# Optimization experiments

Hardware: AMD Instinct MI355X
Metric: run time of the kernel (lower is better)

The kernel has to match this reference:

```python
import jax, jax.numpy as jnp
import numpy as np

B, S, D, H = 2, 4096, 512, 8
HD = D // H
SCALE = HD ** -0.5


def setup_inputs() -> dict:
    key = jax.random.key(0)
    ks = jax.random.split(key, 11)
    std = D ** -0.5
    return {
        "query": jax.random.normal(ks[0], (B, S, D), jnp.float32),
        "key":   jax.random.normal(ks[1], (B, S, D), jnp.float32),
        "value": jax.random.normal(ks[2], (B, S, D), jnp.float32),
        "wq": jax.random.normal(ks[3], (D, D), jnp.float32) * std,
        "bq": jnp.zeros((D,), jnp.float32),
        "wk": jax.random.normal(ks[4], (D, D), jnp.float32) * std,
        "bk": jnp.zeros((D,), jnp.float32),
        "wv": jax.random.normal(ks[5], (D, D), jnp.float32) * std,
        "bv": jnp.zeros((D,), jnp.float32),
        "wo": jax.random.normal(ks[6], (D, D), jnp.float32) * std,
        "bo": jnp.zeros((D,), jnp.float32),
    }


def reference(query, key, value, wq, bq, wk, bk, wv, bv, wo, bo):
    # projections: [B,S,D] -> [B,H,S,HD]
    def split_heads(x):
        return x.reshape(B, S, H, HD).transpose(0, 2, 1, 3)

    q = split_heads(query @ wq + bq)
    k = split_heads(key @ wk + bk)
    v = split_heads(value @ wv + bv)

    # full O(S^2) score matrix, as in the original naive MHA
    scores = jnp.einsum("bhqd,bhkd->bhqk", q, k) * SCALE  # [B,H,S,S]
    attn_weights = jax.nn.softmax(scores, axis=-1)
    attn_output = jnp.einsum("bhqk,bhkd->bhqd", attn_weights, v)
    attn_output = attn_output.transpose(0, 2, 1, 3).reshape(B, S, D)
    attn_output = attn_output @ wo + bo
    return attn_output, attn_weights
```

## Files before the change

### kernel.cpp

```cpp
#include <hip/hip_runtime.h>
#include <hip/hip_bf16.h>
#include <cstdint>
#include <cstddef>

#define B_  2
#define S_  4096
#define D_  512
#define H_  8
#define HD_ 64
#define QSCALE_ 0.18033688f

typedef short s16x8 __attribute__((ext_vector_type(8)));
typedef float f32x4 __attribute__((ext_vector_type(4)));

__device__ __forceinline__ unsigned short f2bf(float f) {
    unsigned u = __builtin_bit_cast(unsigned, f);
    u += 0x7fffu + ((u >> 16) & 1u);
    return (unsigned short)(u >> 16);
}

__device__ __forceinline__ unsigned packbf2(float a, float b) {
    unsigned r;
    asm("v_cvt_pk_bf16_f32 %0, %1, %2" : "=v"(r) : "v"(a), "v"(b));
    return r;
}

__device__ __forceinline__ void gload16(const unsigned short* g, const unsigned short* l) {
    __builtin_amdgcn_global_load_lds(
        (const __attribute__((address_space(1))) void*)g,
        (__attribute__((address_space(3))) void*)l,
        16, 0, 0);
}

__device__ __forceinline__ s16x8 kfr(const unsigned short* buf, int kr, int hb) {
    return *(const s16x8*)((const char*)buf + kr * 128 + (hb ^ ((kr & 7) << 4)));
}
__device__ __forceinline__ s16x8 vfr_(const unsigned short* buf, int vr, int kbyte) {
    return *(const s16x8*)((const char*)buf + vr * 256 + (kbyte ^ ((vr & 15) << 4)));
}

__global__ __launch_bounds__(256)
void prep_weights(const float* __restrict__ wq, const float* __restrict__ wk,
                  const float* __restrict__ wv, const float* __restrict__ wo,
                  unsigned short* __restrict__ wt) {
    int e = blockIdx.x * 256 + threadIdx.x;
    int mat = e >> 18;
    int i = e & 262143;
    int n = i >> 9, k = i & 511;
    const float* w = (mat == 0) ? wq : (mat == 1) ? wk : (mat == 2) ? wv : wo;
    wt[(size_t)mat * 262144 + n * 512 + k] = f2bf(w[k * 512 + n]);
}

__global__ __launch_bounds__(256)
void qkv_gemm(const float* __restrict__ qx, const float* __restrict__ kx,
              const float* __restrict__ vx, const unsigned short* __restrict__ wtb,
              const float* __restrict__ bqp, const float* __restrict__ bkp,
              const float* __restrict__ bvp,
              unsigned short* __restrict__ qo, unsigned short* __restrict__ ko,
              unsigned short* __restrict__ vo) {
    __shared__ unsigned short smem[16384];
    unsigned short* as_ = smem;
    unsigned short* bs_ = smem + 8192;

    const int z = blockIdx.z;
    const float* xin = (z == 0) ? qx : (z == 1) ? kx : vx;
    const unsigned short* wt = wtb + (size_t)z * 262144;
    const float* bias = (z == 0) ? bqp : (z == 1) ? bkp : bvp;
    const float oscale = (z == 0) ? QSCALE_ : 1.0f;

    const int tid  = threadIdx.x;
    const int wave = tid >> 6, lane = tid & 63;
    const int l15 = lane & 15, l4 = lane >> 4;
    const int wr = wave >> 1, wc = wave & 1;
    const int row0 = blockIdx.x * 128, col0 = blockIdx.y * 128;

    const int arow = tid >> 1, ahalf = tid & 1;
    const float* asrc0 = xin + (size_t)(row0 + arow) * 512 + ahalf * 32;

    const int srow = lane >> 3;
    const int scol = 8 * ((lane & 7) ^ srow);
    const unsigned short* bsrc0 = wt + (size_t)(col0 + wave * 32 + srow) * 512 + scol;

    f32x4 acc[4][4] = {};

    for (int kt = 0; kt < 512; kt += 64) {
        #pragma unroll
        for (int i = 0; i < 4; ++i)
            gload16(bsrc0 + (size_t)i * 8 * 512 + kt, bs_ + (wave * 32 + i * 8) * 64);
        {
            const float* a = asrc0 + kt;
            #pragma unroll
            for (int j = 0; j < 4; ++j) {
                float4 v0 = *(const float4*)(a + j * 8);
                float4 v1 = *(const float4*)(a + j * 8 + 4);
                uint4 pk;
                pk.x = packbf2(v0.x, v0.y); pk.y = packbf2(v0.z, v0.w);
                pk.z = packbf2(v1.x, v1.y); pk.w = packbf2(v1.z, v1.w);
                *(uint4*)((char*)as_ + arow * 128 + ((ahalf * 64 + j * 16) ^ ((arow & 7) << 4))) = pk;
            }
        }
        __syncthreads();

        #pragma unroll
        for (int ks = 0; ks < 2; ++ks) {
            s16x8 af[4], bf[4];
            #pragma unroll
            for (int i = 0; i < 4; ++i) {
                af[i] = kfr(as_, wr * 64 + i * 16 + l15, ks * 64 + l4 * 16);
                bf[i] = kfr(bs_, wc * 64 + i * 16 + l15, ks * 64 + l4 * 16);
            }
            #pragma unroll
            for (int mf = 0; mf < 4; ++mf)
                #pragma unroll
                for (int nf = 0; nf < 4; ++nf)
                    acc[mf][nf] = __builtin_amdgcn_mfma_f32_16x16x32_bf16(af[mf], bf[nf], acc[mf][nf], 0, 0, 0);
        }
        __syncthreads();
    }

    if (z == 2) {
        #pragma unroll
        for (int nf = 0; nf < 4; ++nf) {
            const int nl = wc * 64 + nf * 16 + l15;
            float bv = bias[col0 + nl];
            #pragma unroll
            for (int mf = 0; mf < 4; ++mf) {
                uint2 pk;
                pk.x = packbf2(acc[mf][nf][0] + bv, acc[mf][nf][1] + bv);
                pk.y = packbf2(acc[mf][nf][2] + bv, acc[mf][nf][3] + bv);
                int mb = (wr * 64 + mf * 16 + l4 * 4) * 2;
                *(uint2*)((char*)smem + nl * 256 + (mb ^ ((nl & 7) << 4))) = pk;
            }
        }
        __syncthreads();
        const int nl = tid >> 1, half = tid & 1;
        const int c = col0 + nl, hh = c >> 6, hd = c & 63;
        const int bb = row0 >> 12, s0 = row0 & 4095;
        unsigned short* dst = vo + ((size_t)(bb * H_ + hh) * HD_ + hd) * S_ + s0 + half * 64;
        #pragma unroll
        for (int u = 0; u < 8; ++u)
            *(uint4*)((char*)dst + u * 16) =
                *(const uint4*)((char*)smem + nl * 256 + ((half * 128 + u * 16) ^ ((nl & 7) << 4)));
    } else {
        unsigned short* out = (z == 0) ? qo : ko;
        #pragma unroll
        for (int nf = 0; nf < 4; ++nf) {
            int c = col0 + wc * 64 + nf * 16 + l15;
            float bv = bias[c];
            #pragma unroll
            for (int mf = 0; mf < 4; ++mf)
                #pragma unroll
                for (int r = 0; r < 4; ++r) {
                    int t = row0 + wr * 64 + mf * 16 + l4 * 4 + r;
                    out[(size_t)t * 512 + c] = f2bf((acc[mf][nf][r] + bv) * oscale);
                }
        }
    }
}

__global__ __launch_bounds__(256)
void oproj_gemm(const unsigned short* __restrict__ xin, const unsigned short* __restrict__ wt,
                const float* __restrict__ bias, float* __restrict__ out) {
    __shared__ unsigned short xs[64 * 72];
    __shared__ unsigned short wsd[64 * 72];

    const int tid  = threadIdx.x;
    const int wave = tid >> 6, lane = tid & 63;
    const int l15 = lane & 15, l4 = lane >> 4;
    const int row0 = blockIdx.x * 64, col0 = blockIdx.y * 64;
    const int sr = tid >> 2, seg = tid & 3;

    f32x4 acc[4] = {};

    for (int kt = 0; kt < 512; kt += 64) {
        {
            const unsigned short* x = xin + (size_t)(row0 + sr) * 512 + kt + seg * 16;
            *(s16x8*)&xs[sr * 72 + seg * 16]     = *(const s16x8*)(x);
            *(s16x8*)&xs[sr * 72 + seg * 16 + 8] = *(const s16x8*)(x + 8);
        }
        {
            const unsigned short* wp = wt + (size_t)(col0 + sr) * 512 + kt + seg * 16;
            *(s16x8*)&wsd[sr * 72 + seg * 16]     = *(const s16x8*)(wp);
            *(s16x8*)&wsd[sr * 72 + seg * 16 + 8] = *(const s16x8*)(wp + 8);
        }
        __syncthreads();

        #pragma unroll
        for (int ks = 0; ks < 2; ++ks) {
            s16x8 a = *(const s16x8*)&xs[(wave * 16 + l15) * 72 + ks * 32 + l4 * 8];
            #pragma unroll
            for (int ng = 0; ng < 4; ++ng) {
                s16x8 b = *(const s16x8*)&wsd[(ng * 16 + l15) * 72 + ks * 32 + l4 * 8];
                acc[ng] = __builtin_amdgcn_mfma_f32_16x16x32_bf16(a, b, acc[ng], 0, 0, 0);
            }
        }
        __syncthreads();
    }

    #pragma unroll
    for (int ng = 0; ng < 4; ++ng) {
        int c = col0 + ng * 16 + l15;
        float bv = bias[c];
        #pragma unroll
        for (int r = 0; r < 4; ++r) {
            int t = row0 + wave * 16 + l4 * 4 + r;
            out[(size_t)t * 512 + c] = acc[ng][r] + bv;
        }
    }
}

__global__ __launch_bounds__(256)
void attn_kernel(const unsigned short* __restrict__ qb,
                 const unsigned short* __restrict__ kb,
                 const unsigned short* __restrict__ vt,
                 float* __restrict__ wout,
                 unsigned short* __restrict__ ob) {
    __shared__ unsigned short smem[40960];

    const int tid  = threadIdx.x;
    const int wave = tid >> 6, lane = tid & 63;
    const int l15 = lane & 15, l4 = lane >> 4;

    const int lid = blockIdx.x;
    const int wid = (lid & 7) * 64 + (lid >> 3);
    const int bh = wid >> 5;
    const int q0 = (wid & 31) * 128;
    const int b = bh >> 3, h = bh & 7;

    const int ksrow = lane >> 3;
    const int kscol = 8 * ((lane & 7) ^ ksrow);
    const unsigned short* kstg0 = kb + (size_t)(b * S_ + wave * 32 + ksrow) * 512 + h * 64 + kscol;
    const unsigned short* kstg1 = kb + (size_t)(b * S_ + wave * 64 + ksrow) * 512 + h * 64 + kscol;
    const int vsrow = lane >> 4;

#define KSTAGE1(c, bsel)                                                        \
    { _Pragma("unroll")                                                         \
      for (int i_ = 0; i_ < 8; ++i_)                                            \
          gload16(kstg1 + ((size_t)(c) * 256 + i_ * 8) * 512,                   \
                  smem + (bsel) * 16384 + (wave * 64 + i_ * 8) * 64); }

#define KSTAGE(c, bsel)                                                         \
    { _Pragma("unroll")                                                         \
      for (int i_ = 0; i_ < 4; ++i_)                                            \
          gload16(kstg0 + ((size_t)(c) * 128 + i_ * 8) * 512,                   \
                  smem + (bsel) * 8192 + (wave * 32 + i_ * 8) * 64); }

#define VSTAGE(c, bsel)                                                         \
    { _Pragma("unroll")                                                         \
      for (int i_ = 0; i_ < 4; ++i_) {                                          \
          int vrow_ = wave * 16 + i_ * 4 + vsrow;                               \
          int vcb_  = (lane & 15) ^ (i_ * 4 + vsrow);                           \
          gload16(vt + ((size_t)(bh * 64) + vrow_) * 4096 + (c) * 128 + vcb_ * 8, \
                  smem + 16384 + (bsel) * 8192 + (wave * 16 + i_ * 4) * 128); } }

    s16x8 aq[2][2];
    #pragma unroll
    for (int qh = 0; qh < 2; ++qh) {
        const int t = b * S_ + q0 + wave * 32 + qh * 16 + l15;
        const unsigned short* qp = qb + (size_t)t * 512 + h * 64;
        aq[qh][0] = *(const s16x8*)(qp + l4 * 8);
        aq[qh][1] = *(const s16x8*)(qp + 32 + l4 * 8);
    }

    float lsum[2] = {0.0f, 0.0f};
    KSTAGE1(0, 0);
    __syncthreads();

    for (int c = 0; c < 16; ++c) {
        const int cur = c & 1;
        if (c < 15) KSTAGE1(c + 1, cur ^ 1);
        const unsigned short* kcur = smem + cur * 16384;

        #pragma unroll
        for (int sub = 0; sub < 4; ++sub) {
            f32x4 sc[4][2] = {};
            __builtin_amdgcn_s_setprio(1);
            #pragma unroll
            for (int ks = 0; ks < 2; ++ks)
                #pragma unroll
                for (int kg = 0; kg < 4; ++kg) {
                    s16x8 kf = kfr(kcur, sub * 64 + kg * 16 + l15, ks * 64 + l4 * 16);
                    sc[kg][0] = __builtin_amdgcn_mfma_f32_16x16x32_bf16(kf, aq[0][ks], sc[kg][0], 0, 0, 0);
                    sc[kg][1] = __builtin_amdgcn_mfma_f32_16x16x32_bf16(kf, aq[1][ks], sc[kg][1], 0, 0, 0);
                }
            __builtin_amdgcn_s_setprio(0);
            #pragma unroll
            for (int kg = 0; kg < 4; ++kg)
                #pragma unroll
                for (int r = 0; r < 4; ++r) {
                    lsum[0] += __builtin_amdgcn_exp2f(sc[kg][0][r]);
                    lsum[1] += __builtin_amdgcn_exp2f(sc[kg][1][r]);
                }
        }
        __syncthreads();
    }

    #pragma unroll
    for (int qh = 0; qh < 2; ++qh) {
        lsum[qh] += __shfl_xor(lsum[qh], 16);
        lsum[qh] += __shfl_xor(lsum[qh], 32);
    }
    const float off[2] = { -__builtin_amdgcn_logf(lsum[0]),
                           -__builtin_amdgcn_logf(lsum[1]) };

    f32x4 ao[2][4] = {};
    float* wbase = wout + ((size_t)bh * S_ + q0 + wave * 32) * S_;
    unsigned short* strip = smem + 32768 + wave * 2048;

    KSTAGE(0, 0); VSTAGE(0, 0);
    __syncthreads();

    for (int c = 0; c < 32; ++c) {
        const int cur = c & 1;
        if (c < 31) { KSTAGE(c + 1, cur ^ 1); VSTAGE(c + 1, cur ^ 1); }
        const unsigned short* kcur = smem + cur * 8192;
        const unsigned short* vcur = smem + 16384 + cur * 8192;

        #pragma unroll
        for (int sub = 0; sub < 2; ++sub) {
            f32x4 sc[4][2] = {};
            __builtin_amdgcn_s_setprio(1);
            #pragma unroll
            for (int ks = 0; ks < 2; ++ks)
                #pragma unroll
                for (int kg = 0; kg < 4; ++kg) {
                    s16x8 kf = kfr(kcur, sub * 64 + kg * 16 + l15, ks * 64 + l4 * 16);
                    sc[kg][0] = __builtin_amdgcn_mfma_f32_16x16x32_bf16(kf, aq[0][ks], sc[kg][0], 0, 0, 0);
                    sc[kg][1] = __builtin_amdgcn_mfma_f32_16x16x32_bf16(kf, aq[1][ks], sc[kg][1], 0, 0, 0);
                }
            __builtin_amdgcn_s_setprio(0);

            #pragma unroll
            for (int qh = 0; qh < 2; ++qh) {
                float* wrow = wbase + (size_t)(qh * 16 + l15) * S_ + c * 128 + sub * 64;
                const int q = qh * 16 + l15;
                #pragma unroll
                for (int kg = 0; kg < 4; ++kg) {
                    f32x4 w;
                    #pragma unroll
                    for (int r = 0; r < 4; ++r)
                        w[r] = __builtin_amdgcn_exp2f(sc[kg][qh][r] + off[qh]);
                    *(f32x4*)(wrow + kg * 16 + l4 * 4) = w;
                    uint2 pk;
                    pk.x = packbf2(w[0], w[1]);
                    pk.y = packbf2(w[2], w[3]);
                    *(uint2*)((char*)strip + q * 128 + ((kg * 32 + l4 * 8) ^ ((q & 7) << 4))) = pk;
                }
            }

            __builtin_amdgcn_s_setprio(1);
            #pragma unroll
            for (int ks = 0; ks < 2; ++ks) {
                s16x8 pa0 = *(const s16x8*)((const char*)strip + l15 * 128
                               + ((ks * 64 + l4 * 16) ^ ((l15 & 7) << 4)));
                s16x8 pa1 = *(const s16x8*)((const char*)strip + (16 + l15) * 128
                               + ((ks * 64 + l4 * 16) ^ ((l15 & 7) << 4)));
                #pragma unroll
                for (int ng = 0; ng < 4; ++ng) {
                    s16x8 vf = vfr_(vcur, ng * 16 + l15, sub * 128 + ks * 64 + l4 * 16);
                    ao[0][ng] = __builtin_amdgcn_mfma_f32_16x16x32_bf16(pa0, vf, ao[0][ng], 0, 0, 0);
                    ao[1][ng] = __builtin_amdgcn_mfma_f32_16x16x32_bf16(pa1, vf, ao[1][ng], 0, 0, 0);
                }
            }
            __builtin_amdgcn_s_setprio(0);
        }
        __syncthreads();
    }

    #pragma unroll
    for (int qg = 0; qg < 2; ++qg)
        #pragma unroll
        for (int ng = 0; ng < 4; ++ng) {
            int hd = ng * 16 + l15;
            #pragma unroll
            for (int r = 0; r < 4; ++r) {
                int t = b * S_ + q0 + wave * 32 + qg * 16 + l4 * 4 + r;
                ob[(size_t)t * 512 + h * 64 + hd] = f2bf(ao[qg][ng][r]);
            }
        }
#undef KSTAGE1
#undef KSTAGE
#undef VSTAGE
}

extern "C" void kernel_launch(void* const* d_in, const int* in_sizes, int n_in,
                              void* d_out, int out_size, void* d_ws, size_t ws_size,
                              hipStream_t stream) {
    (void)in_sizes; (void)n_in; (void)out_size; (void)ws_size;

    const float* query = (const float*)d_in[0];
    const float* key_  = (const float*)d_in[1];
    const float* value = (const float*)d_in[2];
    const float* wq = (const float*)d_in[3];
    const float* bq = (const float*)d_in[4];
    const float* wk = (const float*)d_in[5];
    const float* bk = (const float*)d_in[6];
    const float* wv = (const float*)d_in[7];
    const float* bv = (const float*)d_in[8];
    const float* wo = (const float*)d_in[9];
    const float* bo = (const float*)d_in[10];
    float* out = (float*)d_out;

    char* ws = (char*)d_ws;
    unsigned short* wt = (unsigned short*)(ws);
    unsigned short* qb = (unsigned short*)(ws + 2097152);
    unsigned short* kb = (unsigned short*)(ws + 2097152 + 1 * 8388608);
    unsigned short* vt = (unsigned short*)(ws + 2097152 + 2 * 8388608);
    unsigned short* ob = (unsigned short*)(ws + 2097152 + 3 * 8388608);

    hipLaunchKernelGGL(prep_weights, dim3(4096), dim3(256), 0, stream, wq, wk, wv, wo, wt);

    hipLaunchKernelGGL(qkv_gemm, dim3(64, 4, 3), dim3(256), 0, stream,
                       query, key_, value, wt, bq, bk, bv, qb, kb, vt);

    hipLaunchKernelGGL(attn_kernel, dim3(512), dim3(256), 0, stream,
                       qb, kb, vt, out + 4194304, ob);

    hipLaunchKernelGGL(oproj_gemm, dim3(128, 8), dim3(256), 0, stream,
                       ob, wt + 3 * 262144, bo, out);
}
```

Before: 350.6 us.

## Tile weight transpose through LDS and enlarge output-projection GEMM tiles

The weight-prep kernel now transposes 64x64 tiles through shared memory with vectorized float4 reads and 16-byte writes, replacing the previous strided per-element gather. The output-projection GEMM moves from 64x64 tiles to 128x128 tiles with 4x4 MFMA fragments per wave, using direct global-to-LDS loads and the swizzled fragment layout already used by the QKV GEMM. This is meant to reduce uncoalesced memory traffic and raise operand reuse, at the cost of fewer blocks (256) for the O-projection and more registers per thread.

```diff
diff --git a/kernel.cpp b/kernel.cpp
--- a/kernel.cpp
+++ b/kernel.cpp
@@ -43,12 +43,32 @@
 void prep_weights(const float* __restrict__ wq, const float* __restrict__ wk,
                   const float* __restrict__ wv, const float* __restrict__ wo,
                   unsigned short* __restrict__ wt) {
-    int e = blockIdx.x * 256 + threadIdx.x;
-    int mat = e >> 18;
-    int i = e & 262143;
-    int n = i >> 9, k = i & 511;
+    __shared__ unsigned short ts[64 * 72];
+
+    const int mat = blockIdx.z;
     const float* w = (mat == 0) ? wq : (mat == 1) ? wk : (mat == 2) ? wv : wo;
-    wt[(size_t)mat * 262144 + n * 512 + k] = f2bf(w[k * 512 + n]);
+    const int k0 = blockIdx.x * 64, n0 = blockIdx.y * 64;
+
+    const int tid = threadIdx.x;
+    const int kr = tid >> 2, nseg = (tid & 3) * 16;
+    {
+        const float* src = w + (size_t)(k0 + kr) * 512 + n0 + nseg;
+        unsigned short tmp[16];
+        #pragma unroll
+        for (int j = 0; j < 16; j += 4) {
+            float4 v = *(const float4*)(src + j);
+            tmp[j] = f2bf(v.x); tmp[j+1] = f2bf(v.y); tmp[j+2] = f2bf(v.z); tmp[j+3] = f2bf(v.w);
+        }
+        #pragma unroll
+        for (int j = 0; j < 16; ++j)
+            ts[(nseg + j) * 72 + kr] = tmp[j];
+    }
+    __syncthreads();
+
+    const int nr = tid >> 2, kseg = (tid & 3) * 16;
+    unsigned short* dst = wt + (size_t)mat * 262144 + (size_t)(n0 + nr) * 512 + k0 + kseg;
+    *(s16x8*)dst       = *(const s16x8*)&ts[nr * 72 + kseg];
+    *(s16x8*)(dst + 8) = *(const s16x8*)&ts[nr * 72 + kseg + 8];
 }
 
 __global__ __launch_bounds__(256)
@@ -161,51 +181,59 @@
 __global__ __launch_bounds__(256)
 void oproj_gemm(const unsigned short* __restrict__ xin, const unsigned short* __restrict__ wt,
                 const float* __restrict__ bias, float* __restrict__ out) {
-    __shared__ unsigned short xs[64 * 72];
-    __shared__ unsigned short wsd[64 * 72];
+    __shared__ unsigned short smem[16384];
+    unsigned short* as_ = smem;
+    unsigned short* bs_ = smem + 8192;
 
     const int tid  = threadIdx.x;
     const int wave = tid >> 6, lane = tid & 63;
     const int l15 = lane & 15, l4 = lane >> 4;
-    const int row0 = blockIdx.x * 64, col0 = blockIdx.y * 64;
-    const int sr = tid >> 2, seg = tid & 3;
-
-    f32x4 acc[4] = {};
+    const int wr = wave >> 1, wc = wave & 1;
+    const int row0 = blockIdx.x * 128, col0 = blockIdx.y * 128;
+
+    const int srow = lane >> 3;
+    const int scol = 8 * ((lane & 7) ^ srow);
+    const unsigned short* asrc0 = xin + (size_t)(row0 + wave * 32 + srow) * 512 + scol;
+    const unsigned short* bsrc0 = wt + (size_t)(col0 + wave * 32 + srow) * 512 + scol;
+
+    f32x4 acc[4][4] = {};
 
     for (int kt = 0; kt < 512; kt += 64) {
-        {
-            const unsigned short* x = xin + (size_t)(row0 + sr) * 512 + kt + seg * 16;
-            *(s16x8*)&xs[sr * 72 + seg * 16]     = *(const s16x8*)(x);
-            *(s16x8*)&xs[sr * 72 + seg * 16 + 8] = *(const s16x8*)(x + 8);
-        }
-        {
-            const unsigned short* wp = wt + (size_t)(col0 + sr) * 512 + kt + seg * 16;
-            *(s16x8*)&wsd[sr * 72 + seg * 16]     = *(const s16x8*)(wp);
-            *(s16x8*)&wsd[sr * 72 + seg * 16 + 8] = *(const s16x8*)(wp + 8);
+        #pragma unroll
+        for (int i = 0; i < 4; ++i) {
+            gload16(asrc0 + (size_t)i * 8 * 512 + kt, as_ + (wave * 32 + i * 8) * 64);
+            gload16(bsrc0 + (size_t)i * 8 * 512 + kt, bs_ + (wave * 32 + i * 8) * 64);
         }
         __syncthreads();
 
         #pragma unroll
         for (int ks = 0; ks < 2; ++ks) {
-            s16x8 a = *(const s16x8*)&xs[(wave * 16 + l15) * 72 + ks * 32 + l4 * 8];
-            #pragma unroll
-            for (int ng = 0; ng < 4; ++ng) {
-                s16x8 b = *(const s16x8*)&wsd[(ng * 16 + l15) * 72 + ks * 32 + l4 * 8];
-                acc[ng] = __builtin_amdgcn_mfma_f32_16x16x32_bf16(a, b, acc[ng], 0, 0, 0);
-            }
+            s16x8 af[4], bf[4];
+            #pragma unroll
+            for (int i = 0; i < 4; ++i) {
+                af[i] = kfr(as_, wr * 64 + i * 16 + l15, ks * 64 + l4 * 16);
+                bf[i] = kfr(bs_, wc * 64 + i * 16 + l15, ks * 64 + l4 * 16);
+            }
+            #pragma unroll
+            for (int mf = 0; mf < 4; ++mf)
+                #pragma unroll
+                for (int nf = 0; nf < 4; ++nf)
+                    acc[mf][nf] = __builtin_amdgcn_mfma_f32_16x16x32_bf16(af[mf], bf[nf], acc[mf][nf], 0, 0, 0);
         }
         __syncthreads();
     }
 
     #pragma unroll
-    for (int ng = 0; ng < 4; ++ng) {
-        int c = col0 + ng * 16 + l15;
+    for (int nf = 0; nf < 4; ++nf) {
+        int c = col0 + wc * 64 + nf * 16 + l15;
         float bv = bias[c];
         #pragma unroll
-        for (int r = 0; r < 4; ++r) {
-            int t = row0 + wave * 16 + l4 * 4 + r;
-            out[(size_t)t * 512 + c] = acc[ng][r] + bv;
-        }
+        for (int mf = 0; mf < 4; ++mf)
+            #pragma unroll
+            for (int r = 0; r < 4; ++r) {
+                int t = row0 + wr * 64 + mf * 16 + l4 * 4 + r;
+                out[(size_t)t * 512 + c] = acc[mf][nf][r] + bv;
+            }
     }
 }
 
@@ -408,7 +436,7 @@
     unsigned short* vt = (unsigned short*)(ws + 2097152 + 2 * 8388608);
     unsigned short* ob = (unsigned short*)(ws + 2097152 + 3 * 8388608);
 
-    hipLaunchKernelGGL(prep_weights, dim3(4096), dim3(256), 0, stream, wq, wk, wv, wo, wt);
+    hipLaunchKernelGGL(prep_weights, dim3(8, 8, 4), dim3(256), 0, stream, wq, wk, wv, wo, wt);
 
     hipLaunchKernelGGL(qkv_gemm, dim3(64, 4, 3), dim3(256), 0, stream,
                        query, key_, value, wt, bq, bk, bv, qb, kb, vt);
@@ -416,6 +444,6 @@
     hipLaunchKernelGGL(attn_kernel, dim3(512), dim3(256), 0, stream,
                        qb, kb, vt, out + 4194304, ob);
 
-    hipLaunchKernelGGL(oproj_gemm, dim3(128, 8), dim3(256), 0, stream,
+    hipLaunchKernelGGL(oproj_gemm, dim3(64, 4), dim3(256), 0, stream,
                        ob, wt + 3 * 262144, bo, out);
 }
```

Result: no change. 347.6 us (-0.9%).
